# Optimization experiments

Hardware: AMD Instinct MI355X
Metric: run time of the kernel (lower is better)

The kernel has to match this reference:

```python
import jax, jax.numpy as jnp
import numpy as np

GAMMA_1 = 4.0
GAMMA_2 = 5.0
EPS = 1e-8  # torch CosineSimilarity default eps

B, D, T, N = 64, 256, 24, 289


def setup_inputs() -> dict:
    key = jax.random.key(0)
    k1, k2 = jax.random.split(key)
    e = jax.random.normal(k1, (B, D, T), dtype=jnp.float32)  # word embeddings [B, D, T]
    v = jax.random.normal(k2, (B, D, N), dtype=jnp.float32)  # region features [B, D, N]
    return {"e": e, "v": v}


def _pair_scores(e, v):
    # Vectorized all-pairs version of batch_score(e[i], v[j]) -> S[i, j]
    # s = e[i].T @ v[j] : [B, B, T, N]
    s = jnp.einsum('idt,jdn->ijtn', e, v)
    s_norm = jax.nn.softmax(s, axis=3)               # softmax over regions (dim=1)
    alpha = jax.nn.softmax(GAMMA_1 * s_norm, axis=2)  # softmax over words (dim=0)
    # c[t, d] = sum_n alpha[t, n] * v[d, n]  -> [B, B, T, D]
    c = jnp.einsum('ijtn,jdn->ijtd', alpha, v)
    # CosineSimilarity(dim=1)(c.t() [D,T], e [D,T]) -> cosine over the T axis, shape [D]
    dot = jnp.einsum('ijtd,idt->ijd', c, e)           # [B, B, D]
    c_norm = jnp.sqrt(jnp.sum(c * c, axis=2))         # [B, B, D]
    e_norm = jnp.sqrt(jnp.sum(e * e, axis=2))         # [B, D]
    R = dot / jnp.maximum(c_norm * e_norm[:, None, :], EPS)
    # log(exp(g2 * R).sum(dim=0)) ** (1/g2), logsumexp over D
    return jnp.power(jax.nn.logsumexp(GAMMA_2 * R, axis=2), 1.0 / GAMMA_2)  # [B, B]


def reference(e, v):
    S = _pair_scores(e, v)          # S[i, j] = batch_score(e[i], v[j])
    batch_sum_score_d = S.sum(axis=1)  # sum_j S[i, j]
    batch_sum_score_q = S.sum(axis=0)  # sum_j S[j, i]
    return (batch_sum_score_d, batch_sum_score_q)
```

## Files before the change

kernel.cpp:

```cpp
#include <hip/hip_runtime.h>
#include <hip/hip_bf16.h>
#include <math.h>

#define BB 64
#define DD 256
#define TT 24
#define NR 289

typedef float f32x4  __attribute__((ext_vector_type(4)));
typedef float f32x16 __attribute__((ext_vector_type(16)));
typedef short bf16x8 __attribute__((ext_vector_type(8)));

#define ETF_OFF  0ul
#define VTF_OFF  1048576ul
#define VB2_OFF  11534336ul
#define EE_OFF   22020096ul
#define SMAT_OFF 23592960ul

__global__ void conv_e_kernel(const float* __restrict__ e,
                              __hip_bfloat16* __restrict__ eTf,
                              float* __restrict__ eE) {
    int i = blockIdx.x, tid = threadIdx.x;
    const float* ei = e + (size_t)i * DD * TT;
    bf16x8* dst = (bf16x8*)eTf + (size_t)i * 1024;
    #pragma unroll
    for (int p = 0; p < 4; ++p) {
        int idx = tid + p * 256;
        int r = idx & 31, sidx = idx >> 5;
        int d0 = sidx * 8;
        __hip_bfloat16 tmp[8];
        #pragma unroll
        for (int q = 0; q < 8; ++q) {
            float f = (r < TT) ? ei[(d0 + q) * TT + r] : 0.f;
            tmp[q] = __float2bfloat16(f);
        }
        dst[idx] = *(bf16x8*)tmp;
    }
    float* dstE = eE + (size_t)i * 6144;
    #pragma unroll
    for (int p = 0; p < 24; ++p) {
        int idx = tid + p * 256;
        int r = idx & 31, rest = idx >> 5;
        int reg = rest % 12, gdt = rest / 12;
        int g2 = gdt & 1, dt = gdt >> 1;
        int t = (reg & 3) + 8 * (reg >> 2) + 4 * g2;
        dstE[idx] = ei[(dt * 32 + r) * TT + t];
    }
}

__global__ __launch_bounds__(256) void conv_v_kernel(const float* __restrict__ v,
                                                     __hip_bfloat16* __restrict__ vTf,
                                                     __hip_bfloat16* __restrict__ vbf2) {
    __shared__ float ld[32][321];
    int j = blockIdx.x >> 3;
    int dbase = (blockIdx.x & 7) * 32;
    int tid = threadIdx.x;
    const float* vj = v + (size_t)j * DD * NR;
    for (int r = 0; r < 32; ++r) {
        const float* row = vj + (size_t)(dbase + r) * NR;
        ld[r][tid] = row[tid];
        if (tid < 64) {
            int n = 256 + tid;
            ld[r][n] = (n < NR) ? row[n] : 0.f;
        }
    }
    __syncthreads();
    {
        bf16x8* dT = (bf16x8*)vTf + (size_t)j * 10240;
        #pragma unroll
        for (int p = 0; p < 5; ++p) {
            int idx = tid + p * 256;
            int r = idx & 31, rest = idx >> 5;
            int nt = rest % 10, sl = rest / 10;
            int sidx = (dbase >> 3) + sl;
            __hip_bfloat16 tmp[8];
            #pragma unroll
            for (int q = 0; q < 8; ++q)
                tmp[q] = __float2bfloat16(ld[sl * 8 + q][nt * 32 + r]);
            dT[(nt * 32 + sidx) * 32 + r] = *(bf16x8*)tmp;
        }
    }
    {
        bf16x8* dB = (bf16x8*)vbf2 + (size_t)j * 10240;
        int dt = dbase >> 5;
        #pragma unroll
        for (int p = 0; p < 5; ++p) {
            int idx = tid + p * 256;
            int r = idx & 31, ks = idx >> 5;
            __hip_bfloat16 tmp[8];
            #pragma unroll
            for (int q = 0; q < 8; ++q)
                tmp[q] = __float2bfloat16(ld[r][ks * 8 + q]);
            dB[(dt * 40 + ks) * 32 + r] = *(bf16x8*)tmp;
        }
    }
}

__global__ __launch_bounds__(256, 6) void pair_kernel(const __hip_bfloat16* __restrict__ eTf,
                                                      const __hip_bfloat16* __restrict__ vTf,
                                                      const __hip_bfloat16* __restrict__ vbf2,
                                                      const float* __restrict__ eE,
                                                      float* __restrict__ Smat) {
    __shared__ __align__(16) __hip_bfloat16 alpha[32 * 320];

    const int tid = threadIdx.x;
    const int wave = tid >> 6, lane = tid & 63;
    const int r = lane & 31, g2 = lane >> 5;
    const int bid = (blockIdx.x & 7) * 512 + (blockIdx.x >> 3);
    const int i = bid & 63, j = bid >> 6;

    char* ab = (char*)alpha;

    {
        uint32_t* rz = (uint32_t*)(ab + 24 * 640);
        #pragma unroll
        for (int q = 0; q < 5; ++q) rz[tid + q * 256] = 0u;
        int t = tid >> 3, n0 = 304 + 2 * (tid & 7);
        int boff = (t * 640 + 2 * n0) ^ ((t & 7) << 4);
        *(uint32_t*)(ab + boff) = 0u;
    }

    const bf16x8* eF = (const bf16x8*)eTf + (size_t)i * 1024;
    const bf16x8* vF = (const bf16x8*)vTf + (size_t)j * 10240;
    #pragma unroll
    for (int ti = 0; ti < 3; ++ti) {
        int nt2 = wave + ti * 4;
        if (nt2 < 10) {
            f32x16 acc;
            #pragma unroll
            for (int z = 0; z < 16; ++z) acc[z] = 0.f;
            int n = nt2 * 32 + r;
            #pragma unroll
            for (int s = 0; s < 16; ++s) {
                bf16x8 af = eF[(s * 2 + g2) * 32 + r];
                bf16x8 bf = vF[(nt2 * 32 + s * 2 + g2) * 32 + r];
                acc = __builtin_amdgcn_mfma_f32_32x32x16_bf16(af, bf, acc, 0, 0, 0);
            }
            if (nt2 < 9 || r < 16) {
                #pragma unroll
                for (int reg = 0; reg < 12; ++reg) {
                    int t = (reg & 3) + 8 * (reg >> 2) + 4 * g2;
                    int boff = (t * 640 + 2 * n) ^ ((t & 7) << 4);
                    *(__hip_bfloat16*)(ab + boff) = __float2bfloat16(acc[reg]);
                }
            }
        }
    }
    __syncthreads();

    #pragma unroll
    for (int tt = 0; tt < 6; ++tt) {
        int t = wave * 6 + tt;
        int base = t * 640, sw = (t & 7) << 4;
        float vls[5];
        #pragma unroll
        for (int k5 = 0; k5 < 5; ++k5) {
            int n = k5 * 64 + lane;
            vls[k5] = (n < NR)
                ? __bfloat162float(*(const __hip_bfloat16*)(ab + ((base + 2 * n) ^ sw)))
                : -INFINITY;
        }
        float m = vls[0];
        #pragma unroll
        for (int k5 = 1; k5 < 5; ++k5) m = fmaxf(m, vls[k5]);
        #pragma unroll
        for (int mk = 32; mk >= 1; mk >>= 1) m = fmaxf(m, __shfl_xor(m, mk, 64));
        float sum = 0.f;
        #pragma unroll
        for (int k5 = 0; k5 < 5; ++k5) { vls[k5] = __expf(vls[k5] - m); sum += vls[k5]; }
        #pragma unroll
        for (int mk = 32; mk >= 1; mk >>= 1) sum += __shfl_xor(sum, mk, 64);
        float inv = 1.f / sum;
        #pragma unroll
        for (int k5 = 0; k5 < 5; ++k5) {
            int n = k5 * 64 + lane;
            if (n < NR)
                *(__hip_bfloat16*)(ab + ((base + 2 * n) ^ sw)) = __float2bfloat16(vls[k5] * inv);
        }
    }
    __syncthreads();

    for (int p = 0; p < 2; ++p) {
        int n = p * 256 + tid;
        if (n < NR) {
            float vals[TT];
            #pragma unroll
            for (int t = 0; t < TT; ++t)
                vals[t] = __bfloat162float(
                    *(const __hip_bfloat16*)(ab + ((t * 640 + 2 * n) ^ ((t & 7) << 4))));
            float m = vals[0];
            #pragma unroll
            for (int t = 1; t < TT; ++t) m = fmaxf(m, vals[t]);
            m *= 4.0f;
            float sum = 0.f;
            #pragma unroll
            for (int t = 0; t < TT; ++t) { vals[t] = __expf(4.0f * vals[t] - m); sum += vals[t]; }
            float inv = 1.f / sum;
            #pragma unroll
            for (int t = 0; t < TT; ++t)
                *(__hip_bfloat16*)(ab + ((t * 640 + 2 * n) ^ ((t & 7) << 4))) =
                    __float2bfloat16(vals[t] * inv);
        }
    }
    __syncthreads();

    const bf16x8* vB2f = (const bf16x8*)vbf2 + (size_t)j * 10240;
    const float* eEp = eE + (size_t)i * 6144;

    float ssum = 0.f;
    #pragma unroll
    for (int ti2 = 0; ti2 < 2; ++ti2) {
        int dt = wave + ti2 * 4;
        f32x16 acc;
        #pragma unroll
        for (int z = 0; z < 16; ++z) acc[z] = 0.f;
        int sw = (r & 7) << 4;
        #pragma unroll
        for (int ks = 0; ks < 20; ++ks) {
            bf16x8 af = *(const bf16x8*)(ab + ((r * 640 + ks * 32 + g2 * 16) ^ sw));
            bf16x8 bf = vB2f[(dt * 40 + ks * 2 + g2) * 32 + r];
            acc = __builtin_amdgcn_mfma_f32_32x32x16_bf16(af, bf, acc, 0, 0, 0);
        }
        float dot = 0.f, cn2 = 0.f, en2 = 0.f;
        #pragma unroll
        for (int reg = 0; reg < 12; ++reg) {
            float ev = eEp[((dt * 2 + g2) * 12 + reg) * 32 + r];
            dot = fmaf(acc[reg], ev, dot);
            cn2 = fmaf(acc[reg], acc[reg], cn2);
            en2 = fmaf(ev, ev, en2);
        }
        dot += __shfl_xor(dot, 32, 64);
        cn2 += __shfl_xor(cn2, 32, 64);
        en2 += __shfl_xor(en2, 32, 64);
        float R = dot / fmaxf(sqrtf(cn2) * sqrtf(en2), 1e-8f);
        ssum += __expf(5.f * R);
    }
    #pragma unroll
    for (int mk = 1; mk <= 32; mk <<= 1) ssum += __shfl_xor(ssum, mk, 64);
    __syncthreads();
    float* red = (float*)alpha;
    if (lane == 0) red[wave] = ssum;
    __syncthreads();
    if (tid == 0) {
        float total = red[0] + red[1] + red[2] + red[3];
        float lse = logf(total * 0.5f);
        Smat[bid] = powf(lse, 0.2f);
    }
}

__global__ void reduce_kernel(const float* __restrict__ Smat, float* __restrict__ out) {
    int k = threadIdx.x;
    float s = 0.f;
    if (k < 64) {
        int i = k;
        for (int j = 0; j < BB; ++j) s += Smat[j * 64 + i];
        out[i] = s;
    } else {
        int jq = k - 64;
        for (int i = 0; i < BB; ++i) s += Smat[jq * 64 + i];
        out[64 + jq] = s;
    }
}

extern "C" void kernel_launch(void* const* d_in, const int* in_sizes, int n_in,
                              void* d_out, int out_size, void* d_ws, size_t ws_size,
                              hipStream_t stream) {
    const float* e = (const float*)d_in[0];
    const float* v = (const float*)d_in[1];
    float* out = (float*)d_out;
    char* ws = (char*)d_ws;
    __hip_bfloat16* eTf  = (__hip_bfloat16*)(ws + ETF_OFF);
    __hip_bfloat16* vTf  = (__hip_bfloat16*)(ws + VTF_OFF);
    __hip_bfloat16* vbf2 = (__hip_bfloat16*)(ws + VB2_OFF);
    float* eE  = (float*)(ws + EE_OFF);
    float* Smat = (float*)(ws + SMAT_OFF);

    conv_e_kernel<<<64, 256, 0, stream>>>(e, eTf, eE);
    conv_v_kernel<<<512, 256, 0, stream>>>(v, vTf, vbf2);
    pair_kernel<<<BB * BB, 256, 0, stream>>>(eTf, vTf, vbf2, eE, Smat);
    reduce_kernel<<<1, 128, 0, stream>>>(Smat, out);
}
```

Baseline: 115.6 us.

## Fuse both softmaxes into registers after the score MFMA, skipping LDS passes

Score accumulators for all three n-tiles stay live in registers. The region softmax is computed with intra-wave shuffles plus a small cross-wave max/sum exchange in shared memory. The word softmax is then done in registers before a single bf16 write of alpha to LDS. This removes the raw-score LDS round trip, two separate softmax passes and a barrier. The cost is higher register pressure, so the launch-bounds occupancy hint drops from 6 to 4 waves.

```diff
diff --git a/kernel.cpp b/kernel.cpp
--- a/kernel.cpp
+++ b/kernel.cpp
@@ -96,12 +96,14 @@
     }
 }
 
-__global__ __launch_bounds__(256, 6) void pair_kernel(const __hip_bfloat16* __restrict__ eTf,
+__global__ __launch_bounds__(256, 4) void pair_kernel(const __hip_bfloat16* __restrict__ eTf,
                                                       const __hip_bfloat16* __restrict__ vTf,
                                                       const __hip_bfloat16* __restrict__ vbf2,
                                                       const float* __restrict__ eE,
                                                       float* __restrict__ Smat) {
     __shared__ __align__(16) __hip_bfloat16 alpha[32 * 320];
+    __shared__ __align__(16) float pm[24][4];
+    __shared__ __align__(16) float ps[24][4];
 
     const int tid = threadIdx.x;
     const int wave = tid >> 6, lane = tid & 63;
@@ -122,88 +124,87 @@
 
     const bf16x8* eF = (const bf16x8*)eTf + (size_t)i * 1024;
     const bf16x8* vF = (const bf16x8*)vTf + (size_t)j * 10240;
+    f32x16 acc[3];
+    #pragma unroll
+    for (int ti = 0; ti < 3; ++ti) {
+        #pragma unroll
+        for (int z = 0; z < 16; ++z) acc[ti][z] = 0.f;
+        int nt2 = wave + ti * 4;
+        if (nt2 < 10) {
+            #pragma unroll
+            for (int s = 0; s < 16; ++s) {
+                bf16x8 af = eF[(s * 2 + g2) * 32 + r];
+                bf16x8 bf = vF[(nt2 * 32 + s * 2 + g2) * 32 + r];
+                acc[ti] = __builtin_amdgcn_mfma_f32_32x32x16_bf16(af, bf, acc[ti], 0, 0, 0);
+            }
+        }
+    }
+
+    float fm[12], fiv[12];
+    #pragma unroll
+    for (int reg = 0; reg < 12; ++reg) {
+        float m = -INFINITY;
+        #pragma unroll
+        for (int ti = 0; ti < 3; ++ti) {
+            int nt2 = wave + ti * 4;
+            bool okn = (nt2 < 9) | ((nt2 == 9) & (r == 0));
+            m = okn ? fmaxf(m, acc[ti][reg]) : m;
+        }
+        #pragma unroll
+        for (int mk = 1; mk <= 16; mk <<= 1) m = fmaxf(m, __shfl_xor(m, mk, 64));
+        float su = 0.f;
+        #pragma unroll
+        for (int ti = 0; ti < 3; ++ti) {
+            int nt2 = wave + ti * 4;
+            bool okn = (nt2 < 9) | ((nt2 == 9) & (r == 0));
+            su += okn ? __expf(acc[ti][reg] - m) : 0.f;
+        }
+        #pragma unroll
+        for (int mk = 1; mk <= 16; mk <<= 1) su += __shfl_xor(su, mk, 64);
+        if (r == 0) {
+            int t = (reg & 3) + 8 * (reg >> 2) + 4 * g2;
+            pm[t][wave] = m; ps[t][wave] = su;
+        }
+    }
+    __syncthreads();
+    #pragma unroll
+    for (int reg = 0; reg < 12; ++reg) {
+        int t = (reg & 3) + 8 * (reg >> 2) + 4 * g2;
+        f32x4 p4 = *(const f32x4*)&pm[t][0];
+        f32x4 q4 = *(const f32x4*)&ps[t][0];
+        float m = fmaxf(fmaxf(p4[0], p4[1]), fmaxf(p4[2], p4[3]));
+        float su = q4[0] * __expf(p4[0] - m) + q4[1] * __expf(p4[1] - m)
+                 + q4[2] * __expf(p4[2] - m) + q4[3] * __expf(p4[3] - m);
+        fm[reg] = m; fiv[reg] = 1.f / su;
+    }
+
     #pragma unroll
     for (int ti = 0; ti < 3; ++ti) {
         int nt2 = wave + ti * 4;
         if (nt2 < 10) {
-            f32x16 acc;
-            #pragma unroll
-            for (int z = 0; z < 16; ++z) acc[z] = 0.f;
+            float ex[12];
+            float colsum = 0.f;
+            #pragma unroll
+            for (int reg = 0; reg < 12; ++reg) {
+                float p = __expf(acc[ti][reg] - fm[reg]) * fiv[reg];
+                float e4 = __expf(4.f * p);
+                ex[reg] = e4; colsum += e4;
+            }
+            colsum += __shfl_xor(colsum, 32, 64);
+            float inv = 1.f / colsum;
             int n = nt2 * 32 + r;
-            #pragma unroll
-            for (int s = 0; s < 16; ++s) {
-                bf16x8 af = eF[(s * 2 + g2) * 32 + r];
-                bf16x8 bf = vF[(nt2 * 32 + s * 2 + g2) * 32 + r];
-                acc = __builtin_amdgcn_mfma_f32_32x32x16_bf16(af, bf, acc, 0, 0, 0);
-            }
             if (nt2 < 9 || r < 16) {
                 #pragma unroll
                 for (int reg = 0; reg < 12; ++reg) {
                     int t = (reg & 3) + 8 * (reg >> 2) + 4 * g2;
                     int boff = (t * 640 + 2 * n) ^ ((t & 7) << 4);
-                    *(__hip_bfloat16*)(ab + boff) = __float2bfloat16(acc[reg]);
+                    *(__hip_bfloat16*)(ab + boff) = __float2bfloat16(ex[reg] * inv);
                 }
             }
         }
     }
     __syncthreads();
 
-    #pragma unroll
-    for (int tt = 0; tt < 6; ++tt) {
-        int t = wave * 6 + tt;
-        int base = t * 640, sw = (t & 7) << 4;
-        float vls[5];
-        #pragma unroll
-        for (int k5 = 0; k5 < 5; ++k5) {
-            int n = k5 * 64 + lane;
-            vls[k5] = (n < NR)
-                ? __bfloat162float(*(const __hip_bfloat16*)(ab + ((base + 2 * n) ^ sw)))
-                : -INFINITY;
-        }
-        float m = vls[0];
-        #pragma unroll
-        for (int k5 = 1; k5 < 5; ++k5) m = fmaxf(m, vls[k5]);
-        #pragma unroll
-        for (int mk = 32; mk >= 1; mk >>= 1) m = fmaxf(m, __shfl_xor(m, mk, 64));
-        float sum = 0.f;
-        #pragma unroll
-        for (int k5 = 0; k5 < 5; ++k5) { vls[k5] = __expf(vls[k5] - m); sum += vls[k5]; }
-        #pragma unroll
-        for (int mk = 32; mk >= 1; mk >>= 1) sum += __shfl_xor(sum, mk, 64);
-        float inv = 1.f / sum;
-        #pragma unroll
-        for (int k5 = 0; k5 < 5; ++k5) {
-            int n = k5 * 64 + lane;
-            if (n < NR)
-                *(__hip_bfloat16*)(ab + ((base + 2 * n) ^ sw)) = __float2bfloat16(vls[k5] * inv);
-        }
-    }
-    __syncthreads();
-
-    for (int p = 0; p < 2; ++p) {
-        int n = p * 256 + tid;
-        if (n < NR) {
-            float vals[TT];
-            #pragma unroll
-            for (int t = 0; t < TT; ++t)
-                vals[t] = __bfloat162float(
-                    *(const __hip_bfloat16*)(ab + ((t * 640 + 2 * n) ^ ((t & 7) << 4))));
-            float m = vals[0];
-            #pragma unroll
-            for (int t = 1; t < TT; ++t) m = fmaxf(m, vals[t]);
-            m *= 4.0f;
-            float sum = 0.f;
-            #pragma unroll
-            for (int t = 0; t < TT; ++t) { vals[t] = __expf(4.0f * vals[t] - m); sum += vals[t]; }
-            float inv = 1.f / sum;
-            #pragma unroll
-            for (int t = 0; t < TT; ++t)
-                *(__hip_bfloat16*)(ab + ((t * 640 + 2 * n) ^ ((t & 7) << 4))) =
-                    __float2bfloat16(vals[t] * inv);
-        }
-    }
-    __syncthreads();
-
     const bf16x8* vB2f = (const bf16x8*)vbf2 + (size_t)j * 10240;
     const float* eEp = eE + (size_t)i * 6144;
 
@@ -211,22 +212,22 @@
     #pragma unroll
     for (int ti2 = 0; ti2 < 2; ++ti2) {
         int dt = wave + ti2 * 4;
-        f32x16 acc;
-        #pragma unroll
-        for (int z = 0; z < 16; ++z) acc[z] = 0.f;
+        f32x16 a2;
+        #pragma unroll
+        for (int z = 0; z < 16; ++z) a2[z] = 0.f;
         int sw = (r & 7) << 4;
         #pragma unroll
         for (int ks = 0; ks < 20; ++ks) {
             bf16x8 af = *(const bf16x8*)(ab + ((r * 640 + ks * 32 + g2 * 16) ^ sw));
             bf16x8 bf = vB2f[(dt * 40 + ks * 2 + g2) * 32 + r];
-            acc = __builtin_amdgcn_mfma_f32_32x32x16_bf16(af, bf, acc, 0, 0, 0);
+            a2 = __builtin_amdgcn_mfma_f32_32x32x16_bf16(af, bf, a2, 0, 0, 0);
         }
         float dot = 0.f, cn2 = 0.f, en2 = 0.f;
         #pragma unroll
         for (int reg = 0; reg < 12; ++reg) {
             float ev = eEp[((dt * 2 + g2) * 12 + reg) * 32 + r];
-            dot = fmaf(acc[reg], ev, dot);
-            cn2 = fmaf(acc[reg], acc[reg], cn2);
+            dot = fmaf(a2[reg], ev, dot);
+            cn2 = fmaf(a2[reg], a2[reg], cn2);
             en2 = fmaf(ev, ev, en2);
         }
         dot += __shfl_xor(dot, 32, 64);
@@ -238,7 +239,7 @@
     #pragma unroll
     for (int mk = 1; mk <= 32; mk <<= 1) ssum += __shfl_xor(ssum, mk, 64);
     __syncthreads();
-    float* red = (float*)alpha;
+    float* red = (float*)pm;
     if (lane == 0) red[wave] = ssum;
     __syncthreads();
     if (tid == 0) {
```

After: 142.3 us. 23.1% more time.
